# Performance work log

Measured on AMD Instinct MI355X. Metric: run time of the kernel, lower is better.

The kernel has to match this reference:

```python
import jax, jax.numpy as jnp
from jax import lax
import numpy as np

B, S, U, T = 128, 512, 1024, 48


def setup_inputs() -> dict:
    key = jax.random.key(0)
    ks = jax.random.split(key, 8)
    H = jax.random.normal(ks[0], (B, S, U), dtype=jnp.float32)
    tag = jax.random.randint(ks[1], (B, S), 0, T, dtype=jnp.int64 if jax.config.read('jax_enable_x64') else jnp.int32)
    s_len = jax.random.randint(ks[2], (B,), 1, S + 1, dtype=tag.dtype)
    w_mask = (jnp.arange(S)[None, :] < s_len[:, None]).astype(jnp.float32)
    # learned params (affine + CRF transitions), per param_init scales
    limit = float(np.sqrt(6.0 / (U + T)))  # xavier_uniform
    W = jax.random.uniform(ks[3], (U, T), minval=-limit, maxval=limit, dtype=jnp.float32)
    b = jnp.zeros((T,), dtype=jnp.float32)
    start_transitions = jax.random.uniform(ks[4], (T,), minval=-0.1, maxval=0.1, dtype=jnp.float32)
    end_transitions = jax.random.uniform(ks[5], (T,), minval=-0.1, maxval=0.1, dtype=jnp.float32)
    transitions = jax.random.uniform(ks[6], (T, T), minval=-0.1, maxval=0.1, dtype=jnp.float32)
    return {"H": H, "W": W, "b": b, "start_transitions": start_transitions,
            "end_transitions": end_transitions, "transitions": transitions,
            "tag": tag, "s_len": s_len, "w_mask": w_mask}


def _crf_log_likelihood(H, W, b, start_transitions, end_transitions, transitions, tag, s_len, w_mask):
    scores = jnp.einsum('bsu,ut->bst', H, W) + b  # (B,S,T) emissions
    # ---- numerator: score of the gold tag path ----
    emit_tag = jnp.take_along_axis(scores, tag[..., None], axis=2)[..., 0]  # (B,S)
    num = start_transitions[tag[:, 0]]
    num = num + jnp.sum(emit_tag * w_mask, axis=1)
    tr = transitions[tag[:, :-1], tag[:, 1:]]  # (B,S-1)
    num = num + jnp.sum(tr * w_mask[:, 1:], axis=1)
    last_tags = jnp.take_along_axis(tag, (s_len - 1)[:, None], axis=1)[:, 0]
    num = num + end_transitions[last_tags]
    # ---- partition: forward algorithm via scan over time ----
    log_prob0 = start_transitions[None, :] + scores[:, 0, :]  # (B,T)

    def step(log_prob, xs):
        emit_i, m_i = xs  # (B,T), (B,)
        # (B,T_prev,1) + (1,T_prev,T_next) + (B,1,T_next) -> lse over T_prev
        new = jax.nn.logsumexp(log_prob[:, :, None] + transitions[None, :, :] + emit_i[:, None, :], axis=1)
        log_prob = jnp.where(m_i[:, None] > 0, new, log_prob)
        return log_prob, None

    xs = (jnp.moveaxis(scores[:, 1:, :], 1, 0), w_mask[:, 1:].T)  # time-major
    log_prob, _ = lax.scan(step, log_prob0, xs)
    log_Z = jax.nn.logsumexp(log_prob + end_transitions[None, :], axis=1)  # (B,)
    return num - log_Z


def reference(H, W, b, start_transitions, end_transitions, transitions, tag, s_len, w_mask):
    return _crf_log_likelihood(H, W, b, start_transitions, end_transitions, transitions, tag, s_len, w_mask)
```

## Files before the change

kernel.cpp:

```cpp
#include <hip/hip_runtime.h>
#include <math.h>

#define B_  128
#define S_  512
#define U_  1024
#define T_  48
#define CHK 32
#define NCH 16
#define PLD 72

typedef short  bf16x8 __attribute__((ext_vector_type(8)));
typedef float  f32x4  __attribute__((ext_vector_type(4)));

__device__ __forceinline__ float rfl(float x) {
    return __int_as_float(__builtin_amdgcn_readfirstlane(__float_as_int(x)));
}
__device__ __forceinline__ unsigned pack_bf16(float lo, float hi) {
    const unsigned a = __float_as_uint(lo) + 0x8000u;
    const unsigned b = __float_as_uint(hi) + 0x8000u;
    return __builtin_amdgcn_perm(b, a, 0x07060302u);
}

__global__ __launch_bounds__(256) void prep_w(
    const float* __restrict__ W, unsigned short* __restrict__ Wt)
{
    const int n = blockIdx.x;
#pragma unroll
    for (int i = 0; i < 4; ++i) {
        const int k = threadIdx.x + 256 * i;
        const unsigned u = __float_as_uint(W[(size_t)k * T_ + n]) + 0x8000u;
        Wt[(size_t)n * U_ + k] = (unsigned short)(u >> 16);
    }
}

#define KC     64
#define HS_LD  72
#define WS_LD  72

__global__ __launch_bounds__(256) void gemm_scores_mfma(
    const float* __restrict__ H, const unsigned short* __restrict__ Wt,
    const float* __restrict__ bias, const int* __restrict__ s_len,
    float* __restrict__ scores)
{
    __shared__ unsigned short Hs[128 * HS_LD];
    __shared__ unsigned short Ws[T_ * WS_LD];

    const int blk = blockIdx.x;
    const int b   = blk >> 2;
    const int s0  = (blk & 3) * 128;
    const int len = s_len[b];
    if (s0 >= len) return;
    const int lim = len - 1 - s0;

    const int tid  = threadIdx.x;
    const int wave = tid >> 6;
    const int lane = tid & 63;
    const int m16  = lane & 15;
    const int q    = lane >> 4;
    const int grp  = tid >> 4;
    const int l16  = tid & 15;

    const size_t row0 = (size_t)b * S_ + s0;
    const float* Hg = H + row0 * U_;

    f32x4 acc[2][3];
#pragma unroll
    for (int mt = 0; mt < 2; ++mt)
#pragma unroll
        for (int nt = 0; nt < 3; ++nt) acc[mt][nt] = (f32x4){0.f, 0.f, 0.f, 0.f};

    for (int kc = 0; kc < U_ / KC; ++kc) {
        const int k0 = kc * KC;
#pragma unroll
        for (int p = 0; p < 8; ++p) {
            const int row = p * 16 + grp;
            const int rl  = row < lim ? row : lim;
            const float4 h = *reinterpret_cast<const float4*>(
                Hg + (size_t)rl * U_ + k0 + l16 * 4);
            const unsigned p01 = pack_bf16(h.x, h.y);
            const unsigned p23 = pack_bf16(h.z, h.w);
            *reinterpret_cast<uint2*>(&Hs[row * HS_LD + l16 * 4]) =
                make_uint2(p01, p23);
        }
#pragma unroll
        for (int i = 0; i < 2; ++i) {
            const int idx = tid + 256 * i;
            if (idx < 384) {
                const int n = idx >> 3, seg = idx & 7;
                const uint4 w = *reinterpret_cast<const uint4*>(
                    Wt + (size_t)n * U_ + k0 + seg * 8);
                *reinterpret_cast<uint4*>(&Ws[n * WS_LD + seg * 8]) = w;
            }
        }
        __syncthreads();

        bf16x8 afr[2][2], bfr[3][2];
#pragma unroll
        for (int mt = 0; mt < 2; ++mt)
#pragma unroll
            for (int ks = 0; ks < 2; ++ks)
                afr[mt][ks] = *reinterpret_cast<const bf16x8*>(
                    &Hs[(wave * 32 + mt * 16 + m16) * HS_LD + ks * 32 + q * 8]);
#pragma unroll
        for (int nt = 0; nt < 3; ++nt)
#pragma unroll
            for (int ks = 0; ks < 2; ++ks)
                bfr[nt][ks] = *reinterpret_cast<const bf16x8*>(
                    &Ws[(nt * 16 + m16) * WS_LD + ks * 32 + q * 8]);
#pragma unroll
        for (int ks = 0; ks < 2; ++ks)
#pragma unroll
            for (int mt = 0; mt < 2; ++mt)
#pragma unroll
                for (int nt = 0; nt < 3; ++nt)
                    acc[mt][nt] = __builtin_amdgcn_mfma_f32_16x16x32_bf16(
                        afr[mt][ks], bfr[nt][ks], acc[mt][nt], 0, 0, 0);
        __syncthreads();
    }

#pragma unroll
    for (int mt = 0; mt < 2; ++mt)
#pragma unroll
        for (int nt = 0; nt < 3; ++nt) {
            const int col = nt * 16 + m16;
            const float bv = bias[col];
#pragma unroll
            for (int i = 0; i < 4; ++i) {
                const size_t r = row0 + wave * 32 + mt * 16 + q * 4 + i;
                scores[r * T_ + col] = acc[mt][nt][i] + bv;
            }
        }
}

__global__ __launch_bounds__(256) void build_ops(
    const float* __restrict__ scores, const float* __restrict__ trans,
    const int* __restrict__ s_len,
    unsigned short* __restrict__ Ptg, float* __restrict__ logS)
{
    __shared__ float Eld[T_ * T_];
    __shared__ __align__(16) unsigned short Pb[4 * 48 * PLD];

    const int tid  = threadIdx.x;
    const int wid  = tid >> 6;
    const int lane = tid & 63;
    const int m16  = lane & 15;
    const int q    = lane >> 4;

    for (int i = tid; i < T_ * T_; i += 256)
        Eld[i] = __expf(trans[i]);
    __syncthreads();

    const int widx = blockIdx.x * 4 + wid;
    const int b    = widx / NCH;
    const int c    = widx % NCH;
    const int len  = s_len[b];
    const int s0   = 1 + c * CHK;
    if (s0 >= len) return;
    const int ns   = (len - s0 < CHK) ? (len - s0) : CHK;

    unsigned short* Ps = &Pb[wid * 48 * PLD];

    bf16x8 afr[3][2];
#pragma unroll
    for (int mt = 0; mt < 3; ++mt)
#pragma unroll
        for (int kt = 0; kt < 2; ++kt) {
            union { bf16x8 v; unsigned short s[8]; } u;
#pragma unroll
            for (int j = 0; j < 8; ++j) {
                const int k = kt * 32 + q * 8 + j;
                const int m = mt * 16 + m16;
                const float ev = (k < T_) ? Eld[k * T_ + m] : 0.f;
                u.s[j] = (unsigned short)((__float_as_uint(ev) + 0x8000u) >> 16);
            }
            afr[mt][kt] = u.v;
        }

    {
        uint4* p4 = reinterpret_cast<uint4*>(Ps);
        const uint4 z = make_uint4(0u, 0u, 0u, 0u);
        for (int i = lane; i < 48 * PLD / 8; i += 64) p4[i] = z;
        __builtin_amdgcn_wave_barrier();
        if (lane < T_) Ps[lane * PLD + lane] = 0x3F80;
        __builtin_amdgcn_wave_barrier();
    }

    const float* sb = scores + ((size_t)b * S_ + s0) * T_;
    float logacc = 0.f;

    float4 emld[3];
#pragma unroll
    for (int mt = 0; mt < 3; ++mt)
        emld[mt] = reinterpret_cast<const float4*>(sb)[mt * 4 + q];

    for (int i = 0; i < ns; ++i) {
        float4 em[3];
#pragma unroll
        for (int mt = 0; mt < 3; ++mt) {
            em[mt].x = __expf(emld[mt].x); em[mt].y = __expf(emld[mt].y);
            em[mt].z = __expf(emld[mt].z); em[mt].w = __expf(emld[mt].w);
        }
        if (i + 1 < ns) {
            const float* sn = sb + (i + 1) * T_;
#pragma unroll
            for (int mt = 0; mt < 3; ++mt)
                emld[mt] = reinterpret_cast<const float4*>(sn)[mt * 4 + q];
        }

        bf16x8 bfr[2][3];
#pragma unroll
        for (int kt = 0; kt < 2; ++kt)
#pragma unroll
            for (int nt = 0; nt < 3; ++nt)
                bfr[kt][nt] = *reinterpret_cast<const bf16x8*>(
                    &Ps[(nt * 16 + m16) * PLD + kt * 32 + q * 8]);

        f32x4 acc[3][3];
#pragma unroll
        for (int mt = 0; mt < 3; ++mt)
#pragma unroll
            for (int nt = 0; nt < 3; ++nt) acc[mt][nt] = (f32x4){0.f,0.f,0.f,0.f};
#pragma unroll
        for (int kt = 0; kt < 2; ++kt)
#pragma unroll
            for (int mt = 0; mt < 3; ++mt)
#pragma unroll
                for (int nt = 0; nt < 3; ++nt)
                    acc[mt][nt] = __builtin_amdgcn_mfma_f32_16x16x32_bf16(
                        afr[mt][kt], bfr[kt][nt], acc[mt][nt], 0, 0, 0);

        const float r    = rfl(acc[0][0][0] * em[0].x);
        const float rinv = __builtin_amdgcn_rcpf(r);
        logacc += __logf(r);
        __builtin_amdgcn_wave_barrier();
#pragma unroll
        for (int mt = 0; mt < 3; ++mt) {
            const float sx = em[mt].x * rinv, sy = em[mt].y * rinv;
            const float sz = em[mt].z * rinv, sw = em[mt].w * rinv;
#pragma unroll
            for (int nt = 0; nt < 3; ++nt) {
                const unsigned lo = pack_bf16(acc[mt][nt][0] * sx,
                                              acc[mt][nt][1] * sy);
                const unsigned hi = pack_bf16(acc[mt][nt][2] * sz,
                                              acc[mt][nt][3] * sw);
                *reinterpret_cast<uint2*>(
                    &Ps[(nt * 16 + m16) * PLD + mt * 16 + q * 4]) =
                    make_uint2(lo, hi);
            }
        }
        __builtin_amdgcn_wave_barrier();
    }

    if (lane < T_) {
        unsigned outp[24];
#pragma unroll
        for (int j2 = 0; j2 < 24; ++j2) {
            const unsigned a  = Ps[(2 * j2)     * PLD + lane];
            const unsigned b2 = Ps[(2 * j2 + 1) * PLD + lane];
            outp[j2] = a | (b2 << 16);
        }
        unsigned short* dst =
            Ptg + (((size_t)b * NCH + c) * 48 + lane) * 48;
        uint4* d4 = reinterpret_cast<uint4*>(dst);
#pragma unroll
        for (int t4 = 0; t4 < 6; ++t4)
            d4[t4] = make_uint4(outp[4*t4], outp[4*t4+1],
                                outp[4*t4+2], outp[4*t4+3]);
    }
    if (lane == 0) logS[(size_t)b * NCH + c] = logacc;
}

__global__ __launch_bounds__(64) void crf_forward(
    const float* __restrict__ scores, const unsigned short* __restrict__ Ptg,
    const float* __restrict__ logS,
    const float* __restrict__ start_tr, const float* __restrict__ end_tr,
    const float* __restrict__ trans, const int* __restrict__ tag,
    const int* __restrict__ s_len, float* __restrict__ out)
{
    __shared__ float Tr[T_ * T_];
    __shared__ __align__(16) float wb[2][64];

    const int b    = blockIdx.x;
    const int lane = threadIdx.x;

    for (int i = lane; i < T_ * T_; i += 64)
        Tr[i] = trans[i];
    __syncthreads();

    const int len = s_len[b];
    const float* sc = scores + (size_t)b * S_ * T_;
    const int*   tg = tag + (size_t)b * S_;

    float nsum = 0.f;
    for (int s = lane; s < len; s += 64) {
        const int t = tg[s];
        nsum += sc[s * T_ + t];
        if (s >= 1) nsum += Tr[tg[s - 1] * T_ + t];
    }
#pragma unroll
    for (int off = 32; off >= 1; off >>= 1)
        nsum += __shfl_xor(nsum, off);

    const int col = (lane < T_) ? lane : 0;

    const float lp0 = (lane < T_) ? (start_tr[lane] + sc[lane]) : -1e30f;
    const float m0  = rfl(lp0);
    float v = __expf(lp0 - m0);
    float C = m0;
    float invr = 1.0f, lr = 0.0f;
    int par = 0;

    const int F = (len - 1 + CHK - 1) / CHK;
    const unsigned short* Pb_ = Ptg + (size_t)b * NCH * 48 * 48;
    const float* Lb = logS + (size_t)b * NCH;

    uint4 cur[6], nxt[6];
    float ls_cur = 0.f, ls_nxt = 0.f;
    if (F > 0) {
        const uint4* p = reinterpret_cast<const uint4*>(Pb_ + (size_t)col * 48);
#pragma unroll
        for (int i = 0; i < 6; ++i) cur[i] = p[i];
        ls_cur = Lb[0];
    }
    for (int cc = 0; cc < F; ++cc) {
        if (cc + 1 < F) {
            const uint4* p = reinterpret_cast<const uint4*>(
                Pb_ + (size_t)(cc + 1) * 2304 + (size_t)col * 48);
#pragma unroll
            for (int i = 0; i < 6; ++i) nxt[i] = p[i];
            ls_nxt = Lb[cc + 1];
        }
        float pr[48];
#pragma unroll
        for (int i = 0; i < 6; ++i) {
            const uint4 u = cur[i];
            pr[8*i+0] = __uint_as_float(u.x << 16);
            pr[8*i+1] = __uint_as_float(u.x & 0xFFFF0000u);
            pr[8*i+2] = __uint_as_float(u.y << 16);
            pr[8*i+3] = __uint_as_float(u.y & 0xFFFF0000u);
            pr[8*i+4] = __uint_as_float(u.z << 16);
            pr[8*i+5] = __uint_as_float(u.z & 0xFFFF0000u);
            pr[8*i+6] = __uint_as_float(u.w << 16);
            pr[8*i+7] = __uint_as_float(u.w & 0xFFFF0000u);
        }
        wb[par & 1][lane] = v;
        __builtin_amdgcn_wave_barrier();
        const float4* a4 = reinterpret_cast<const float4*>(wb[par & 1]);
        float d0=0.f,d1=0.f,d2=0.f,d3=0.f,d4=0.f,d5=0.f,d6=0.f,d7=0.f;
#pragma unroll
        for (int j4 = 0; j4 < 6; ++j4) {
            const float4 pa = a4[2 * j4];
            const float4 pb = a4[2 * j4 + 1];
            d0 = fmaf(pa.x, pr[8*j4+0], d0);
            d1 = fmaf(pa.y, pr[8*j4+1], d1);
            d2 = fmaf(pa.z, pr[8*j4+2], d2);
            d3 = fmaf(pa.w, pr[8*j4+3], d3);
            d4 = fmaf(pb.x, pr[8*j4+4], d4);
            d5 = fmaf(pb.y, pr[8*j4+5], d5);
            d6 = fmaf(pb.z, pr[8*j4+6], d6);
            d7 = fmaf(pb.w, pr[8*j4+7], d7);
        }
        __builtin_amdgcn_wave_barrier();
        const float dt = ((d0 + d4) + (d1 + d5)) + ((d2 + d6) + (d3 + d7));
        v = dt * invr;
        C += lr + ls_cur;
        const float r = rfl(v);
        invr = __builtin_amdgcn_rcpf(r);
        lr   = __logf(r);
        par ^= 1;
#pragma unroll
        for (int i = 0; i < 6; ++i) cur[i] = nxt[i];
        ls_cur = ls_nxt;
    }

    float z = (lane < T_) ? v * __expf(end_tr[lane]) : 0.f;
#pragma unroll
    for (int off = 32; off >= 1; off >>= 1)
        z += __shfl_xor(z, off);
    const float logZ = C + __logf(z);

    if (lane == 0) {
        const float num = nsum + start_tr[tg[0]] + end_tr[tg[len - 1]];
        out[b] = num - logZ;
    }
}

extern "C" void kernel_launch(void* const* d_in, const int* in_sizes, int n_in,
                              void* d_out, int out_size, void* d_ws, size_t ws_size,
                              hipStream_t stream) {
    const float* H        = (const float*)d_in[0];
    const float* W        = (const float*)d_in[1];
    const float* bias     = (const float*)d_in[2];
    const float* start_tr = (const float*)d_in[3];
    const float* end_tr   = (const float*)d_in[4];
    const float* trans    = (const float*)d_in[5];
    const int*   tag      = (const int*)d_in[6];
    const int*   s_len    = (const int*)d_in[7];

    const size_t NSC = (size_t)B_ * S_ * T_;
    float*          scores = (float*)d_ws;
    float*          logS   = scores + NSC;
    unsigned short* Wt     = (unsigned short*)(logS + B_ * NCH);
    unsigned short* Ptg    = Wt + (size_t)T_ * U_;

    hipLaunchKernelGGL(prep_w, dim3(T_), dim3(256), 0, stream, W, Wt);
    hipLaunchKernelGGL(gemm_scores_mfma, dim3((B_ * S_) / 128), dim3(256), 0,
                       stream, H, Wt, bias, s_len, scores);
    hipLaunchKernelGGL(build_ops, dim3(B_ * NCH / 4), dim3(256), 0, stream,
                       scores, trans, s_len, Ptg, logS);
    hipLaunchKernelGGL(crf_forward, dim3(B_), dim3(64), 0, stream,
                       scores, Ptg, logS, start_tr, end_tr, trans, tag, s_len,
                       (float*)d_out);
}
```

Measured before the change: 412.0 us.

## Register-prefetch GEMM tiles and triple-buffer CRF chunk loads

The scores GEMM now loads the next K-chunk of H and W into registers before converting and storing the current chunk to LDS, so global loads overlap with the MFMA work. It also sets launch_bounds occupancy to 2 blocks. The CRF forward kernel now uses three register buffers, prefetching two chunks ahead instead of one, to hide global latency in the serial chain. Both changes raise register pressure, which could cut occupancy or cause spills.

```diff
diff --git a/kernel.cpp b/kernel.cpp
--- a/kernel.cpp
+++ b/kernel.cpp
@@ -37,7 +37,67 @@
 #define HS_LD  72
 #define WS_LD  72
 
-__global__ __launch_bounds__(256) void gemm_scores_mfma(
+#define G_ISSUE(kc, H_, W_)                                              \
+    {                                                                    \
+        const int k0_ = (kc) * KC;                                       \
+        _Pragma("unroll")                                                \
+        for (int p = 0; p < 8; ++p) {                                    \
+            const int row_ = p * 16 + grp;                               \
+            const int rl_  = row_ < lim ? row_ : lim;                    \
+            H_[p] = *reinterpret_cast<const float4*>(                    \
+                Hg + (size_t)rl_ * U_ + k0_ + l16 * 4);                  \
+        }                                                                \
+        W_[0] = *reinterpret_cast<const uint4*>(                         \
+            Wt + (size_t)(tid >> 3) * U_ + k0_ + (tid & 7) * 8);         \
+        if (tid < 128)                                                   \
+            W_[1] = *reinterpret_cast<const uint4*>(                     \
+                Wt + (size_t)((tid + 256) >> 3) * U_ + k0_ +             \
+                (tid & 7) * 8);                                          \
+    }
+
+#define G_STEP(kc, H_, W_, HN_, WN_)                                     \
+    {                                                                    \
+        if ((kc) + 1 < U_ / KC) G_ISSUE((kc) + 1, HN_, WN_);             \
+        _Pragma("unroll")                                                \
+        for (int p = 0; p < 8; ++p) {                                    \
+            const int row_ = p * 16 + grp;                               \
+            const unsigned p01 = pack_bf16(H_[p].x, H_[p].y);            \
+            const unsigned p23 = pack_bf16(H_[p].z, H_[p].w);            \
+            *reinterpret_cast<uint2*>(&Hs[row_ * HS_LD + l16 * 4]) =     \
+                make_uint2(p01, p23);                                    \
+        }                                                                \
+        *reinterpret_cast<uint4*>(                                       \
+            &Ws[(tid >> 3) * WS_LD + (tid & 7) * 8]) = W_[0];            \
+        if (tid < 128)                                                   \
+            *reinterpret_cast<uint4*>(                                   \
+                &Ws[((tid + 256) >> 3) * WS_LD + (tid & 7) * 8]) = W_[1];\
+        __syncthreads();                                                 \
+        bf16x8 afr[2][2], bfr[3][2];                                     \
+        _Pragma("unroll")                                                \
+        for (int mt = 0; mt < 2; ++mt)                                   \
+            _Pragma("unroll")                                            \
+            for (int ks = 0; ks < 2; ++ks)                               \
+                afr[mt][ks] = *reinterpret_cast<const bf16x8*>(          \
+                    &Hs[(wave * 32 + mt * 16 + m16) * HS_LD +            \
+                        ks * 32 + q * 8]);                               \
+        _Pragma("unroll")                                                \
+        for (int nt = 0; nt < 3; ++nt)                                   \
+            _Pragma("unroll")                                            \
+            for (int ks = 0; ks < 2; ++ks)                               \
+                bfr[nt][ks] = *reinterpret_cast<const bf16x8*>(          \
+                    &Ws[(nt * 16 + m16) * WS_LD + ks * 32 + q * 8]);     \
+        _Pragma("unroll")                                                \
+        for (int ks = 0; ks < 2; ++ks)                                   \
+            _Pragma("unroll")                                            \
+            for (int mt = 0; mt < 2; ++mt)                               \
+                _Pragma("unroll")                                        \
+                for (int nt = 0; nt < 3; ++nt)                           \
+                    acc[mt][nt] = __builtin_amdgcn_mfma_f32_16x16x32_bf16(\
+                        afr[mt][ks], bfr[nt][ks], acc[mt][nt], 0, 0, 0); \
+        __syncthreads();                                                 \
+    }
+
+__global__ __launch_bounds__(256, 2) void gemm_scores_mfma(
     const float* __restrict__ H, const unsigned short* __restrict__ Wt,
     const float* __restrict__ bias, const int* __restrict__ s_len,
     float* __restrict__ scores)
@@ -69,53 +129,13 @@
 #pragma unroll
         for (int nt = 0; nt < 3; ++nt) acc[mt][nt] = (f32x4){0.f, 0.f, 0.f, 0.f};
 
-    for (int kc = 0; kc < U_ / KC; ++kc) {
-        const int k0 = kc * KC;
-#pragma unroll
-        for (int p = 0; p < 8; ++p) {
-            const int row = p * 16 + grp;
-            const int rl  = row < lim ? row : lim;
-            const float4 h = *reinterpret_cast<const float4*>(
-                Hg + (size_t)rl * U_ + k0 + l16 * 4);
-            const unsigned p01 = pack_bf16(h.x, h.y);
-            const unsigned p23 = pack_bf16(h.z, h.w);
-            *reinterpret_cast<uint2*>(&Hs[row * HS_LD + l16 * 4]) =
-                make_uint2(p01, p23);
-        }
-#pragma unroll
-        for (int i = 0; i < 2; ++i) {
-            const int idx = tid + 256 * i;
-            if (idx < 384) {
-                const int n = idx >> 3, seg = idx & 7;
-                const uint4 w = *reinterpret_cast<const uint4*>(
-                    Wt + (size_t)n * U_ + k0 + seg * 8);
-                *reinterpret_cast<uint4*>(&Ws[n * WS_LD + seg * 8]) = w;
-            }
-        }
-        __syncthreads();
-
-        bf16x8 afr[2][2], bfr[3][2];
-#pragma unroll
-        for (int mt = 0; mt < 2; ++mt)
-#pragma unroll
-            for (int ks = 0; ks < 2; ++ks)
-                afr[mt][ks] = *reinterpret_cast<const bf16x8*>(
-                    &Hs[(wave * 32 + mt * 16 + m16) * HS_LD + ks * 32 + q * 8]);
-#pragma unroll
-        for (int nt = 0; nt < 3; ++nt)
-#pragma unroll
-            for (int ks = 0; ks < 2; ++ks)
-                bfr[nt][ks] = *reinterpret_cast<const bf16x8*>(
-                    &Ws[(nt * 16 + m16) * WS_LD + ks * 32 + q * 8]);
-#pragma unroll
-        for (int ks = 0; ks < 2; ++ks)
-#pragma unroll
-            for (int mt = 0; mt < 2; ++mt)
-#pragma unroll
-                for (int nt = 0; nt < 3; ++nt)
-                    acc[mt][nt] = __builtin_amdgcn_mfma_f32_16x16x32_bf16(
-                        afr[mt][ks], bfr[nt][ks], acc[mt][nt], 0, 0, 0);
-        __syncthreads();
+    float4 ha[8], hb[8];
+    uint4  wa[2], wb2[2];
+
+    G_ISSUE(0, ha, wa);
+    for (int kc = 0; kc < U_ / KC; kc += 2) {
+        G_STEP(kc,     ha, wa,  hb, wb2);
+        G_STEP(kc + 1, hb, wb2, ha, wa);
     }
 
 #pragma unroll
@@ -270,6 +290,58 @@
     if (lane == 0) logS[(size_t)b * NCH + c] = logacc;
 }
 
+#define LOADCH(dst, lsdst, idx)                                          \
+    {                                                                    \
+        const uint4* p_ = reinterpret_cast<const uint4*>(                \
+            Pb_ + (size_t)(idx) * 2304 + (size_t)col * 48);              \
+        _Pragma("unroll")                                                \
+        for (int i_ = 0; i_ < 6; ++i_) dst[i_] = p_[i_];                 \
+        lsdst = Lb[idx];                                                 \
+    }
+
+#define CRF_BODY(CUR, CL, N2, N2L, CC)                                   \
+    {                                                                    \
+        if ((CC) + 2 < F) LOADCH(N2, N2L, (CC) + 2);                     \
+        float pr[48];                                                    \
+        _Pragma("unroll")                                                \
+        for (int i_ = 0; i_ < 6; ++i_) {                                 \
+            const uint4 u = CUR[i_];                                     \
+            pr[8*i_+0] = __uint_as_float(u.x << 16);                     \
+            pr[8*i_+1] = __uint_as_float(u.x & 0xFFFF0000u);             \
+            pr[8*i_+2] = __uint_as_float(u.y << 16);                     \
+            pr[8*i_+3] = __uint_as_float(u.y & 0xFFFF0000u);             \
+            pr[8*i_+4] = __uint_as_float(u.z << 16);                     \
+            pr[8*i_+5] = __uint_as_float(u.z & 0xFFFF0000u);             \
+            pr[8*i_+6] = __uint_as_float(u.w << 16);                     \
+            pr[8*i_+7] = __uint_as_float(u.w & 0xFFFF0000u);             \
+        }                                                                \
+        wb[par & 1][lane] = v;                                           \
+        __builtin_amdgcn_wave_barrier();                                 \
+        const float4* a4 = reinterpret_cast<const float4*>(wb[par & 1]); \
+        float d0=0.f,d1=0.f,d2=0.f,d3=0.f,d4=0.f,d5=0.f,d6=0.f,d7=0.f;   \
+        _Pragma("unroll")                                                \
+        for (int j4 = 0; j4 < 6; ++j4) {                                 \
+            const float4 pa = a4[2 * j4];                                \
+            const float4 pb = a4[2 * j4 + 1];                            \
+            d0 = fmaf(pa.x, pr[8*j4+0], d0);                             \
+            d1 = fmaf(pa.y, pr[8*j4+1], d1);                             \
+            d2 = fmaf(pa.z, pr[8*j4+2], d2);                             \
+            d3 = fmaf(pa.w, pr[8*j4+3], d3);                             \
+            d4 = fmaf(pb.x, pr[8*j4+4], d4);                             \
+            d5 = fmaf(pb.y, pr[8*j4+5], d5);                             \
+            d6 = fmaf(pb.z, pr[8*j4+6], d6);                             \
+            d7 = fmaf(pb.w, pr[8*j4+7], d7);                             \
+        }                                                                \
+        __builtin_amdgcn_wave_barrier();                                 \
+        const float dt = ((d0 + d4) + (d1 + d5)) + ((d2 + d6) + (d3 + d7));\
+        v = dt * invr;                                                   \
+        C += lr + CL;                                                    \
+        const float r_ = rfl(v);                                         \
+        invr = __builtin_amdgcn_rcpf(r_);                                \
+        lr   = __logf(r_);                                               \
+        par ^= 1;                                                        \
+    }
+
 __global__ __launch_bounds__(64) void crf_forward(
     const float* __restrict__ scores, const unsigned short* __restrict__ Ptg,
     const float* __restrict__ logS,
@@ -314,63 +386,21 @@
     const unsigned short* Pb_ = Ptg + (size_t)b * NCH * 48 * 48;
     const float* Lb = logS + (size_t)b * NCH;
 
-    uint4 cur[6], nxt[6];
-    float ls_cur = 0.f, ls_nxt = 0.f;
-    if (F > 0) {
-        const uint4* p = reinterpret_cast<const uint4*>(Pb_ + (size_t)col * 48);
-#pragma unroll
-        for (int i = 0; i < 6; ++i) cur[i] = p[i];
-        ls_cur = Lb[0];
-    }
-    for (int cc = 0; cc < F; ++cc) {
-        if (cc + 1 < F) {
-            const uint4* p = reinterpret_cast<const uint4*>(
-                Pb_ + (size_t)(cc + 1) * 2304 + (size_t)col * 48);
-#pragma unroll
-            for (int i = 0; i < 6; ++i) nxt[i] = p[i];
-            ls_nxt = Lb[cc + 1];
-        }
-        float pr[48];
-#pragma unroll
-        for (int i = 0; i < 6; ++i) {
-            const uint4 u = cur[i];
-            pr[8*i+0] = __uint_as_float(u.x << 16);
-            pr[8*i+1] = __uint_as_float(u.x & 0xFFFF0000u);
-            pr[8*i+2] = __uint_as_float(u.y << 16);
-            pr[8*i+3] = __uint_as_float(u.y & 0xFFFF0000u);
-            pr[8*i+4] = __uint_as_float(u.z << 16);
-            pr[8*i+5] = __uint_as_float(u.z & 0xFFFF0000u);
-            pr[8*i+6] = __uint_as_float(u.w << 16);
-            pr[8*i+7] = __uint_as_float(u.w & 0xFFFF0000u);
-        }
-        wb[par & 1][lane] = v;
-        __builtin_amdgcn_wave_barrier();
-        const float4* a4 = reinterpret_cast<const float4*>(wb[par & 1]);
-        float d0=0.f,d1=0.f,d2=0.f,d3=0.f,d4=0.f,d5=0.f,d6=0.f,d7=0.f;
-#pragma unroll
-        for (int j4 = 0; j4 < 6; ++j4) {
-            const float4 pa = a4[2 * j4];
-            const float4 pb = a4[2 * j4 + 1];
-            d0 = fmaf(pa.x, pr[8*j4+0], d0);
-            d1 = fmaf(pa.y, pr[8*j4+1], d1);
-            d2 = fmaf(pa.z, pr[8*j4+2], d2);
-            d3 = fmaf(pa.w, pr[8*j4+3], d3);
-            d4 = fmaf(pb.x, pr[8*j4+4], d4);
-            d5 = fmaf(pb.y, pr[8*j4+5], d5);
-            d6 = fmaf(pb.z, pr[8*j4+6], d6);
-            d7 = fmaf(pb.w, pr[8*j4+7], d7);
-        }
-        __builtin_amdgcn_wave_barrier();
-        const float dt = ((d0 + d4) + (d1 + d5)) + ((d2 + d6) + (d3 + d7));
-        v = dt * invr;
-        C += lr + ls_cur;
-        const float r = rfl(v);
-        invr = __builtin_amdgcn_rcpf(r);
-        lr   = __logf(r);
-        par ^= 1;
-#pragma unroll
-        for (int i = 0; i < 6; ++i) cur[i] = nxt[i];
-        ls_cur = ls_nxt;
+    uint4 c0[6], c1[6], c2[6];
+    float l0_ = 0.f, l1_ = 0.f, l2_ = 0.f;
+    if (F > 0) LOADCH(c0, l0_, 0);
+    if (F > 1) LOADCH(c1, l1_, 1);
+
+    int cc = 0;
+    while (cc + 3 <= F) {
+        CRF_BODY(c0, l0_, c2, l2_, cc);
+        CRF_BODY(c1, l1_, c0, l0_, cc + 1);
+        CRF_BODY(c2, l2_, c1, l1_, cc + 2);
+        cc += 3;
+    }
+    if (cc < F) {
+        CRF_BODY(c0, l0_, c2, l2_, cc); ++cc;
+        if (cc < F) { CRF_BODY(c1, l1_, c0, l0_, cc); ++cc; }
     }
 
     float z = (lane < T_) ? v * __expf(end_tr[lane]) : 0.f;
```

New measurement: 420.4 us. +2.0%, slower.
